# Performance work log

Measured on AMD Instinct MI355X. Metric: run time of the kernel, lower is better.

Reference implementation:

```python
import jax, jax.numpy as jnp
import numpy as np

N, M, D = 32768, 8192, 64

def setup_inputs() -> dict:
    key = jax.random.key(0)
    k1, k2, k3 = jax.random.split(key, 3)
    inputx = jax.random.normal(k1, (N, D), dtype=jnp.float32)
    y = jax.random.normal(k2, (M, D), dtype=jnp.float32)
    # psi is initialized to zeros in the module, but use random values so the
    # dual-variable subtraction actually affects the argmin/min.
    psi = jax.random.normal(k3, (M,), dtype=jnp.float32)
    return {"inputx": inputx, "y": y, "psi": psi}

def reference(inputx, y, psi):
    # cxy[i,j] = ||x_i||^2 + ||y_j||^2 - 2 <x_i, y_j>   (squared euclidean cost)
    x2 = jnp.sum(inputx * inputx, axis=1, keepdims=True)          # [N,1]
    y2 = jnp.sum(y * y, axis=1)[None, :]                          # [1,M]
    cxy = x2 + y2 - 2.0 * jnp.matmul(inputx, y.T)                 # [N,M]
    # semi-dual: mean_i min_j (c(x_i,y_j) - psi_j) + mean_j psi_j
    loss = jnp.mean(jnp.min(cxy - psi[None, :], axis=1)) + jnp.mean(psi)
    return loss
```

## Files before the change

### kernel.cpp

```cpp
#include <hip/hip_runtime.h>

#define N_ROWS 32768
#define M_COLS 8192
#define D_DIM  64
#define JC     8
#define PBLOCK 256
#define BLOCK  256
#define RBLOCK 128
#define GROUPS 2
#define ROWS_PER_BLOCK 256
#define CHUNK  (M_COLS / JC)
#define TJ     128
#define NTILE  (CHUNK / TJ)

typedef _Float16 v8h  __attribute__((ext_vector_type(8)));
typedef _Float16 v4h  __attribute__((ext_vector_type(4)));
typedef float    v4f  __attribute__((ext_vector_type(4)));
typedef float    v16f __attribute__((ext_vector_type(16)));

__global__ __launch_bounds__(PBLOCK) void prep_kernel(
    const float* __restrict__ y, const float* __restrict__ psi,
    const float* __restrict__ x, _Float16* __restrict__ yh,
    float* __restrict__ th, _Float16* __restrict__ xh,
    float* __restrict__ x2, float* __restrict__ out) {
    const int tid = threadIdx.x;
    const int bid = blockIdx.x;
    const int n = tid & 15;
    if (bid < M_COLS / 16) {
        if (bid == 0 && tid == 0) out[0] = 0.f;
        const int j = bid * 16 + (tid >> 4);
        const float4 v = *(const float4*)(y + (size_t)j * D_DIM + n * 4);
        float s = v.x * v.x + v.y * v.y + v.z * v.z + v.w * v.w;
        v4h hv = { (_Float16)v.x, (_Float16)v.y, (_Float16)v.z, (_Float16)v.w };
        *(v4h*)(yh + (size_t)j * D_DIM + n * 4) = hv;
#pragma unroll
        for (int m = 1; m < 16; m <<= 1) s += __shfl_xor(s, m, 64);
        if (n == 0) th[j] = 0.5f * (psi[j] - s);
    } else {
        const int i = (bid - M_COLS / 16) * 16 + (tid >> 4);
        const float4 v = *(const float4*)(x + (size_t)i * D_DIM + n * 4);
        float s = v.x * v.x + v.y * v.y + v.z * v.z + v.w * v.w;
        v4h hv = { (_Float16)v.x, (_Float16)v.y, (_Float16)v.z, (_Float16)v.w };
        *(v4h*)(xh + (size_t)i * D_DIM + n * 4) = hv;
#pragma unroll
        for (int m = 1; m < 16; m <<= 1) s += __shfl_xor(s, m, 64);
        if (n == 0) x2[i] = s;
    }
}

__global__ __launch_bounds__(BLOCK, 4) void partial_min_kernel(
    const _Float16* __restrict__ xh, const _Float16* __restrict__ yh,
    const float* __restrict__ th, float* __restrict__ part) {
    __shared__ __align__(16) _Float16 sY[2][TJ * D_DIM];
    __shared__ __align__(16) float    sTh[2][TJ];

    const int tid  = threadIdx.x;
    const int lane = tid & 63, wave = tid >> 6;
    const int hi = lane >> 5, r32 = lane & 31;
    const int jc    = blockIdx.y;
    const int jbase = jc * CHUNK;
    const int i_wave = blockIdx.x * ROWS_PER_BLOCK + wave * 64;

    auto stage = [&](int t, int b) {
#pragma unroll
        for (int k = 0; k < 4; ++k) {
            const int sIdx = (k * 4 + wave) * 64 + lane;
            const int row  = sIdx >> 3;
            const int c    = (sIdx & 7) ^ (row & 7);
            const _Float16* g = yh + (size_t)(jbase + t * TJ + row) * D_DIM + c * 8;
            __builtin_amdgcn_global_load_lds(
                (const __attribute__((address_space(1))) void*)g,
                (__attribute__((address_space(3))) void*)(&sY[b][(size_t)(k * 4 + wave) * 512]),
                16, 0, 0);
        }
        if (wave == 0 && lane < 32) {
            const float* gt_ = th + (size_t)(jbase + t * TJ) + lane * 4;
            __builtin_amdgcn_global_load_lds(
                (const __attribute__((address_space(1))) void*)gt_,
                (__attribute__((address_space(3))) void*)(&sTh[b][0]),
                16, 0, 0);
        }
    };

    stage(0, 0);

    v8h b[GROUPS][4];
#pragma unroll
    for (int g = 0; g < GROUPS; ++g) {
        const _Float16* px = xh + (size_t)(i_wave + g * 32 + r32) * D_DIM + hi * 8;
#pragma unroll
        for (int ks = 0; ks < 4; ++ks) b[g][ks] = *(const v8h*)(px + ks * 16);
    }

    float maxs[GROUPS];
#pragma unroll
    for (int g = 0; g < GROUPS; ++g) maxs[g] = -INFINITY;

    int aoff0 = r32 * 128 + (((0 * 2 + hi) ^ (r32 & 7)) * 16);
    int aoff1 = r32 * 128 + (((1 * 2 + hi) ^ (r32 & 7)) * 16);
    int aoff2 = r32 * 128 + (((2 * 2 + hi) ^ (r32 & 7)) * 16);
    int aoff3 = r32 * 128 + (((3 * 2 + hi) ^ (r32 & 7)) * 16);

    __syncthreads();

    for (int t = 0; t < NTILE; ++t) {
        const int cur = t & 1;
        if (t + 1 < NTILE) stage(t + 1, cur ^ 1);

        const char*  buf  = (const char*)&sY[cur][0];
        const float* tbuf = &sTh[cur][0];
#pragma unroll
        for (int jb = 0; jb < TJ / 32; ++jb) {
            const v8h a0 = *(const v8h*)(buf + jb * 4096 + aoff0);
            const v8h a1 = *(const v8h*)(buf + jb * 4096 + aoff1);
            const v8h a2 = *(const v8h*)(buf + jb * 4096 + aoff2);
            const v8h a3 = *(const v8h*)(buf + jb * 4096 + aoff3);
            const v4f tq0 = *(const v4f*)(tbuf + jb * 32 + hi * 4);
            const v4f tq1 = *(const v4f*)(tbuf + jb * 32 + hi * 4 + 8);
            const v4f tq2 = *(const v4f*)(tbuf + jb * 32 + hi * 4 + 16);
            const v4f tq3 = *(const v4f*)(tbuf + jb * 32 + hi * 4 + 24);
            v16f cin;
#pragma unroll
            for (int e = 0; e < 4; ++e) {
                cin[e]      = tq0[e];
                cin[e + 4]  = tq1[e];
                cin[e + 8]  = tq2[e];
                cin[e + 12] = tq3[e];
            }
#pragma unroll
            for (int g = 0; g < GROUPS; ++g) {
                v16f acc = __builtin_amdgcn_mfma_f32_32x32x16_f16(a0, b[g][0], cin, 0, 0, 0);
                acc = __builtin_amdgcn_mfma_f32_32x32x16_f16(a1, b[g][1], acc, 0, 0, 0);
                acc = __builtin_amdgcn_mfma_f32_32x32x16_f16(a2, b[g][2], acc, 0, 0, 0);
                acc = __builtin_amdgcn_mfma_f32_32x32x16_f16(a3, b[g][3], acc, 0, 0, 0);
                const float m0 = fmaxf(fmaxf(acc[0],  acc[1]),  fmaxf(acc[2],  acc[3]));
                const float m1 = fmaxf(fmaxf(acc[4],  acc[5]),  fmaxf(acc[6],  acc[7]));
                const float m2 = fmaxf(fmaxf(acc[8],  acc[9]),  fmaxf(acc[10], acc[11]));
                const float m3 = fmaxf(fmaxf(acc[12], acc[13]), fmaxf(acc[14], acc[15]));
                maxs[g] = fmaxf(maxs[g], fmaxf(fmaxf(m0, m1), fmaxf(m2, m3)));
            }
        }
        __syncthreads();
    }

#pragma unroll
    for (int g = 0; g < GROUPS; ++g) {
        float v = maxs[g];
        v = fmaxf(v, __shfl_xor(v, 32, 64));
        if (hi == 0)
            part[(size_t)jc * N_ROWS + i_wave + g * 32 + r32] = -2.f * v;
    }
}

__global__ __launch_bounds__(RBLOCK) void reduce_kernel(
    const float* __restrict__ part, const float* __restrict__ x2,
    const float* __restrict__ psi, float* __restrict__ out) {
    const int tid = threadIdx.x;
    const int gt  = blockIdx.x * RBLOCK + tid;
    float m = part[gt];
#pragma unroll
    for (int c = 1; c < JC; ++c)
        m = fminf(m, part[(size_t)c * N_ROWS + gt]);
    float s = (m + x2[gt]) * (1.f / (float)N_ROWS);
    if (gt < M_COLS) s += psi[gt] * (1.f / (float)M_COLS);
    for (int off = 32; off > 0; off >>= 1) s += __shfl_down(s, off, 64);
    __shared__ float tmp[2];
    if ((tid & 63) == 0) tmp[tid >> 6] = s;
    __syncthreads();
    if (tid == 0) atomicAdd(out, tmp[0] + tmp[1]);
}

extern "C" void kernel_launch(void* const* d_in, const int* in_sizes, int n_in,
                              void* d_out, int out_size, void* d_ws, size_t ws_size,
                              hipStream_t stream) {
    const float* x   = (const float*)d_in[0];
    const float* y   = (const float*)d_in[1];
    const float* psi = (const float*)d_in[2];
    float* out = (float*)d_out;

    float* part = (float*)d_ws;
    float* th   = part + (size_t)JC * N_ROWS;
    float* x2   = th + (size_t)M_COLS;
    _Float16* yh = (_Float16*)(x2 + (size_t)N_ROWS);
    _Float16* xh = yh + (size_t)M_COLS * D_DIM;

    prep_kernel<<<(M_COLS + N_ROWS) / 16, PBLOCK, 0, stream>>>(y, psi, x, yh, th, xh, x2, out);
    partial_min_kernel<<<dim3(N_ROWS / ROWS_PER_BLOCK, JC), BLOCK, 0, stream>>>(xh, yh, th, part);
    reduce_kernel<<<N_ROWS / RBLOCK, RBLOCK, 0, stream>>>(part, x2, psi, out);
}
```

Measured before the change: 103.8 us.

## Swap MFMA operand roles, widen row groups, defer max reduction to epilogue

```diff
diff --git a/kernel.cpp b/kernel.cpp
--- a/kernel.cpp
+++ b/kernel.cpp
@@ -7,8 +7,8 @@
 #define PBLOCK 256
 #define BLOCK  256
 #define RBLOCK 128
-#define GROUPS 2
-#define ROWS_PER_BLOCK 256
+#define GROUPS 4
+#define ROWS_PER_BLOCK 512
 #define CHUNK  (M_COLS / JC)
 #define TJ     128
 #define NTILE  (CHUNK / TJ)
@@ -48,7 +48,7 @@
     }
 }
 
-__global__ __launch_bounds__(BLOCK, 4) void partial_min_kernel(
+__global__ __launch_bounds__(BLOCK, 2) void partial_min_kernel(
     const _Float16* __restrict__ xh, const _Float16* __restrict__ yh,
     const float* __restrict__ th, float* __restrict__ part) {
     __shared__ __align__(16) _Float16 sY[2][TJ * D_DIM];
@@ -59,7 +59,7 @@
     const int hi = lane >> 5, r32 = lane & 31;
     const int jc    = blockIdx.y;
     const int jbase = jc * CHUNK;
-    const int i_wave = blockIdx.x * ROWS_PER_BLOCK + wave * 64;
+    const int i_wave = blockIdx.x * ROWS_PER_BLOCK + wave * (GROUPS * 32);
 
     auto stage = [&](int t, int b) {
 #pragma unroll
@@ -84,22 +84,24 @@
 
     stage(0, 0);
 
-    v8h b[GROUPS][4];
+    v8h a[GROUPS][4];
 #pragma unroll
     for (int g = 0; g < GROUPS; ++g) {
         const _Float16* px = xh + (size_t)(i_wave + g * 32 + r32) * D_DIM + hi * 8;
 #pragma unroll
-        for (int ks = 0; ks < 4; ++ks) b[g][ks] = *(const v8h*)(px + ks * 16);
+        for (int ks = 0; ks < 4; ++ks) a[g][ks] = *(const v8h*)(px + ks * 16);
     }
 
-    float maxs[GROUPS];
+    v16f vmax[GROUPS];
 #pragma unroll
-    for (int g = 0; g < GROUPS; ++g) maxs[g] = -INFINITY;
+    for (int g = 0; g < GROUPS; ++g)
+#pragma unroll
+        for (int e = 0; e < 16; ++e) vmax[g][e] = -INFINITY;
 
-    int aoff0 = r32 * 128 + (((0 * 2 + hi) ^ (r32 & 7)) * 16);
-    int aoff1 = r32 * 128 + (((1 * 2 + hi) ^ (r32 & 7)) * 16);
-    int aoff2 = r32 * 128 + (((2 * 2 + hi) ^ (r32 & 7)) * 16);
-    int aoff3 = r32 * 128 + (((3 * 2 + hi) ^ (r32 & 7)) * 16);
+    const int boff0 = r32 * 128 + (((0 * 2 + hi) ^ (r32 & 7)) * 16);
+    const int boff1 = r32 * 128 + (((1 * 2 + hi) ^ (r32 & 7)) * 16);
+    const int boff2 = r32 * 128 + (((2 * 2 + hi) ^ (r32 & 7)) * 16);
+    const int boff3 = r32 * 128 + (((3 * 2 + hi) ^ (r32 & 7)) * 16);
 
     __syncthreads();
 
@@ -111,44 +113,46 @@
         const float* tbuf = &sTh[cur][0];
 #pragma unroll
         for (int jb = 0; jb < TJ / 32; ++jb) {
-            const v8h a0 = *(const v8h*)(buf + jb * 4096 + aoff0);
-            const v8h a1 = *(const v8h*)(buf + jb * 4096 + aoff1);
-            const v8h a2 = *(const v8h*)(buf + jb * 4096 + aoff2);
-            const v8h a3 = *(const v8h*)(buf + jb * 4096 + aoff3);
-            const v4f tq0 = *(const v4f*)(tbuf + jb * 32 + hi * 4);
-            const v4f tq1 = *(const v4f*)(tbuf + jb * 32 + hi * 4 + 8);
-            const v4f tq2 = *(const v4f*)(tbuf + jb * 32 + hi * 4 + 16);
-            const v4f tq3 = *(const v4f*)(tbuf + jb * 32 + hi * 4 + 24);
+            const v8h b0 = *(const v8h*)(buf + jb * 4096 + boff0);
+            const v8h b1 = *(const v8h*)(buf + jb * 4096 + boff1);
+            const v8h b2 = *(const v8h*)(buf + jb * 4096 + boff2);
+            const v8h b3 = *(const v8h*)(buf + jb * 4096 + boff3);
+            const float tl = tbuf[jb * 32 + r32];
             v16f cin;
 #pragma unroll
-            for (int e = 0; e < 4; ++e) {
-                cin[e]      = tq0[e];
-                cin[e + 4]  = tq1[e];
-                cin[e + 8]  = tq2[e];
-                cin[e + 12] = tq3[e];
-            }
+            for (int e = 0; e < 16; ++e) cin[e] = tl;
+            __builtin_amdgcn_s_setprio(1);
 #pragma unroll
             for (int g = 0; g < GROUPS; ++g) {
-                v16f acc = __builtin_amdgcn_mfma_f32_32x32x16_f16(a0, b[g][0], cin, 0, 0, 0);
-                acc = __builtin_amdgcn_mfma_f32_32x32x16_f16(a1, b[g][1], acc, 0, 0, 0);
-                acc = __builtin_amdgcn_mfma_f32_32x32x16_f16(a2, b[g][2], acc, 0, 0, 0);
-                acc = __builtin_amdgcn_mfma_f32_32x32x16_f16(a3, b[g][3], acc, 0, 0, 0);
-                const float m0 = fmaxf(fmaxf(acc[0],  acc[1]),  fmaxf(acc[2],  acc[3]));
-                const float m1 = fmaxf(fmaxf(acc[4],  acc[5]),  fmaxf(acc[6],  acc[7]));
-                const float m2 = fmaxf(fmaxf(acc[8],  acc[9]),  fmaxf(acc[10], acc[11]));
-                const float m3 = fmaxf(fmaxf(acc[12], acc[13]), fmaxf(acc[14], acc[15]));
-                maxs[g] = fmaxf(maxs[g], fmaxf(fmaxf(m0, m1), fmaxf(m2, m3)));
+                v16f acc = __builtin_amdgcn_mfma_f32_32x32x16_f16(a[g][0], b0, cin, 0, 0, 0);
+                acc = __builtin_amdgcn_mfma_f32_32x32x16_f16(a[g][1], b1, acc, 0, 0, 0);
+                acc = __builtin_amdgcn_mfma_f32_32x32x16_f16(a[g][2], b2, acc, 0, 0, 0);
+                acc = __builtin_amdgcn_mfma_f32_32x32x16_f16(a[g][3], b3, acc, 0, 0, 0);
+#pragma unroll
+                for (int e = 0; e < 16; ++e)
+                    vmax[g][e] = fmaxf(vmax[g][e], acc[e]);
             }
+            __builtin_amdgcn_s_setprio(0);
         }
         __syncthreads();
     }
 
 #pragma unroll
     for (int g = 0; g < GROUPS; ++g) {
-        float v = maxs[g];
-        v = fmaxf(v, __shfl_xor(v, 32, 64));
-        if (hi == 0)
-            part[(size_t)jc * N_ROWS + i_wave + g * 32 + r32] = -2.f * v;
+#pragma unroll
+        for (int e = 0; e < 16; ++e) {
+            float v = vmax[g][e];
+#pragma unroll
+            for (int m = 1; m < 32; m <<= 1)
+                v = fmaxf(v, __shfl_xor(v, m, 64));
+            vmax[g][e] = v;
+        }
+        float v = vmax[g][0];
+#pragma unroll
+        for (int e = 1; e < 16; ++e) v = (r32 == e) ? vmax[g][e] : v;
+        if (r32 < 16)
+            part[(size_t)jc * N_ROWS + i_wave + g * 32
+                 + (r32 & 3) + 8 * (r32 >> 2) + 4 * hi] = -2.f * v;
     }
 }
 
```

Result: slower. 115.4 us (+11.2%).
